# Performance work log

Measured on AMD Instinct MI355X. Metric: run time of the kernel, lower is better.

## Reference

```python
import jax, jax.numpy as jnp
import numpy as np
from jax import lax

DIM = 1024
B, N = 4, 4096


def setup_inputs() -> dict:
    key = jax.random.key(0)
    k1, k2 = jax.random.split(key)
    x = jax.random.normal(k1, (B, N, DIM), dtype=jnp.float32)
    # Linear(dim, 3*dim, bias=False): weight stored as [3*dim, dim] (torch convention)
    w_qkva = jax.random.normal(k2, (3 * DIM, DIM), dtype=jnp.float32) * (DIM ** -0.5)
    gamma = jnp.ones((DIM,), dtype=jnp.float32)  # RMSNorm gain
    return {"x": x, "w_qkva": w_qkva, "gamma": gamma}


def _rmsnorm(x, gamma):
    # lucidrains RMSNorm: F.normalize(x, dim=-1) * sqrt(dim) * gamma
    scale = jnp.asarray(x.shape[-1], x.dtype) ** 0.5
    norm = jnp.sqrt(jnp.sum(x * x, axis=-1, keepdims=True))
    return x / jnp.maximum(norm, 1e-12) * scale * gamma


def reference(x, w_qkva, gamma):
    h = _rmsnorm(x, gamma)                                  # [b, n, d]
    qkva = jnp.einsum('bnd,ed->bne', h, w_qkva)             # [b, n, 3d]
    q, kv, a = jnp.split(qkva, 3, axis=-1)                  # each [b, n, d]
    a = jax.nn.sigmoid(a)

    def binary_operator(e_i, e_j):
        a_i, kv_i = e_i
        a_j, kv_j = e_j
        return (a_j * a_i, a_j * kv_i + kv_j)

    # gated linear recurrence over the sequence axis (elementwise per channel)
    _, y = lax.associative_scan(binary_operator, (a, kv), axis=1)
    return q * y                                            # [b, n, d]
```

## Files before the change

kernel.cpp:

```cpp
#include <hip/hip_runtime.h>
#include <hip/hip_bf16.h>

#define SEQ_N 4096
#define BATCH 4
#define DIM 1024
#define M_ROWS (BATCH * SEQ_N)
#define NCOLS (3 * DIM)
#define KDIM DIM
#define CHUNK_L 16
#define NCHUNK (SEQ_N / CHUNK_L)
#define NCHANNEL (BATCH * DIM)

using short8 = __attribute__((ext_vector_type(8))) short;
using f32x4  = __attribute__((ext_vector_type(4))) float;

static __device__ __forceinline__ unsigned short f2bf(float f) {
    union { float f; unsigned u; } v; v.f = f;
    unsigned r = v.u + 0x7fffu + ((v.u >> 16) & 1u);
    return (unsigned short)(r >> 16);
}
static __device__ __forceinline__ float bf2f(unsigned short s) {
    union { unsigned u; float f; } v; v.u = ((unsigned)s) << 16;
    return v.f;
}

__global__ __launch_bounds__(256) void prep_kernel(const float* __restrict__ x,
                                                   const float* __restrict__ gamma,
                                                   unsigned short* __restrict__ h,
                                                   const float* __restrict__ w,
                                                   unsigned short* __restrict__ wb) {
    if (blockIdx.x < 4096) {
        const int wave = threadIdx.x >> 6;
        const int lane = threadIdx.x & 63;
        const int row = blockIdx.x * 4 + wave;
        const float4* xr = reinterpret_cast<const float4*>(x + (size_t)row * DIM);
        const float4* gr = reinterpret_cast<const float4*>(gamma);
        float4 v[4];
        float ss = 0.f;
#pragma unroll
        for (int i = 0; i < 4; ++i) {
            v[i] = xr[i * 64 + lane];
            ss += v[i].x * v[i].x + v[i].y * v[i].y + v[i].z * v[i].z + v[i].w * v[i].w;
        }
#pragma unroll
        for (int off = 32; off >= 1; off >>= 1) ss += __shfl_xor(ss, off, 64);
        const float scale = 32.0f / fmaxf(sqrtf(ss), 1e-12f);
        ushort4* hr = reinterpret_cast<ushort4*>(h + (size_t)row * DIM);
#pragma unroll
        for (int i = 0; i < 4; ++i) {
            float4 g = gr[i * 64 + lane];
            ushort4 o;
            o.x = f2bf(v[i].x * scale * g.x);
            o.y = f2bf(v[i].y * scale * g.y);
            o.z = f2bf(v[i].z * scale * g.z);
            o.w = f2bf(v[i].w * scale * g.w);
            hr[i * 64 + lane] = o;
        }
    } else {
        const int i = (blockIdx.x - 4096) * 256 + threadIdx.x;
        float4 vv = reinterpret_cast<const float4*>(w)[i];
        ushort4 o;
        o.x = f2bf(vv.x); o.y = f2bf(vv.y); o.z = f2bf(vv.z); o.w = f2bf(vv.w);
        reinterpret_cast<ushort4*>(wb)[i] = o;
    }
}

__global__ __launch_bounds__(256) void gemm_bt_kernel(const unsigned short* __restrict__ A,
                                                      const unsigned short* __restrict__ B,
                                                      unsigned short* __restrict__ C) {
    __shared__ __align__(16) unsigned short sA[128 * 32];
    __shared__ __align__(16) unsigned short sB[128 * 32];

    const int tid  = threadIdx.x;
    const int lane = tid & 63;
    const int wave = tid >> 6;
    const int row0 = blockIdx.y * 128;
    const int col0 = blockIdx.x * 128;
    const int wm = (wave >> 1) * 64;
    const int wn = (wave & 1) * 64;
    const int fr = lane & 15;
    const int kq = lane >> 4;

    const unsigned short* agp = A + (size_t)(row0 + (tid >> 2)) * KDIM + (tid & 3) * 8;
    const unsigned short* bgp = B + (size_t)(col0 + (tid >> 2)) * KDIM + (tid & 3) * 8;

    f32x4 acc[4][4] = {};

    for (int k0 = 0; k0 < KDIM; k0 += 32) {
        __builtin_amdgcn_global_load_lds(
            (const __attribute__((address_space(1))) void*)(agp),
            (__attribute__((address_space(3))) void*)(&sA[tid * 8]), 16, 0, 0);
        __builtin_amdgcn_global_load_lds(
            (const __attribute__((address_space(1))) void*)(agp + 64 * KDIM),
            (__attribute__((address_space(3))) void*)(&sA[2048 + tid * 8]), 16, 0, 0);
        __builtin_amdgcn_global_load_lds(
            (const __attribute__((address_space(1))) void*)(bgp),
            (__attribute__((address_space(3))) void*)(&sB[tid * 8]), 16, 0, 0);
        __builtin_amdgcn_global_load_lds(
            (const __attribute__((address_space(1))) void*)(bgp + 64 * KDIM),
            (__attribute__((address_space(3))) void*)(&sB[2048 + tid * 8]), 16, 0, 0);
        agp += 32; bgp += 32;
        __syncthreads();

        short8 af[4], bf[4];
#pragma unroll
        for (int i = 0; i < 4; ++i)
            af[i] = *reinterpret_cast<const short8*>(&sA[(wm + i * 16 + fr) * 32 + kq * 8]);
#pragma unroll
        for (int j = 0; j < 4; ++j)
            bf[j] = *reinterpret_cast<const short8*>(&sB[(wn + j * 16 + fr) * 32 + kq * 8]);
#pragma unroll
        for (int i = 0; i < 4; ++i)
#pragma unroll
            for (int j = 0; j < 4; ++j)
                acc[i][j] = __builtin_amdgcn_mfma_f32_16x16x32_bf16(af[i], bf[j], acc[i][j], 0, 0, 0);
        __syncthreads();
    }

#pragma unroll
    for (int i = 0; i < 4; ++i) {
#pragma unroll
        for (int j = 0; j < 4; ++j) {
#pragma unroll
            for (int r = 0; r < 4; ++r) {
                int row = row0 + wm + i * 16 + kq * 4 + r;
                int col = col0 + wn + j * 16 + fr;
                C[(size_t)row * NCOLS + col] = f2bf(acc[i][j][r]);
            }
        }
    }
}

__global__ __launch_bounds__(256) void chunk_agg_kernel(const unsigned short* __restrict__ qkva,
                                                        float2* __restrict__ AY) {
    const int c = blockIdx.x, b = blockIdx.y;
    const int d4 = threadIdx.x;
    const unsigned short* base = qkva + ((size_t)b * SEQ_N + c * CHUNK_L) * NCOLS;
    float s[4] = {0.f, 0.f, 0.f, 0.f};
    float A[4] = {1.f, 1.f, 1.f, 1.f};
#pragma unroll 4
    for (int n = 0; n < CHUNK_L; ++n) {
        ushort4 kv4 = reinterpret_cast<const ushort4*>(base + (size_t)n * NCOLS + DIM)[d4];
        ushort4 av4 = reinterpret_cast<const ushort4*>(base + (size_t)n * NCOLS + 2 * DIM)[d4];
        float kv[4] = {bf2f(kv4.x), bf2f(kv4.y), bf2f(kv4.z), bf2f(kv4.w)};
        float av[4] = {bf2f(av4.x), bf2f(av4.y), bf2f(av4.z), bf2f(av4.w)};
#pragma unroll
        for (int t = 0; t < 4; ++t) {
            float a = 1.f / (1.f + __expf(-av[t]));
            s[t] = a * s[t] + kv[t];
            A[t] *= a;
        }
    }
    float4* o = reinterpret_cast<float4*>(AY + (size_t)c * NCHANNEL + b * DIM);
    float4 p0, p1;
    p0.x = A[0]; p0.y = s[0]; p0.z = A[1]; p0.w = s[1];
    p1.x = A[2]; p1.y = s[2]; p1.z = A[3]; p1.w = s[3];
    o[2 * d4]     = p0;
    o[2 * d4 + 1] = p1;
}

__global__ __launch_bounds__(64) void agg_scan_kernel(const float2* __restrict__ AY,
                                                      float* __restrict__ Sin) {
    const int ch = blockIdx.x * 64 + threadIdx.x;
    float s = 0.f;
#pragma unroll 8
    for (int c = 0; c < NCHUNK; ++c) {
        Sin[(size_t)c * NCHANNEL + ch] = s;
        float2 ay = AY[(size_t)c * NCHANNEL + ch];
        s = ay.x * s + ay.y;
    }
}

__global__ __launch_bounds__(256) void apply_kernel(const unsigned short* __restrict__ qkva,
                                                    const float* __restrict__ Sin,
                                                    float* __restrict__ out) {
    const int c = blockIdx.x, b = blockIdx.y;
    const int d4 = threadIdx.x;
    const unsigned short* base = qkva + ((size_t)b * SEQ_N + c * CHUNK_L) * NCOLS;
    float* obase = out + ((size_t)b * SEQ_N + c * CHUNK_L) * DIM;
    float4 s4 = reinterpret_cast<const float4*>(Sin + (size_t)c * NCHANNEL + b * DIM)[d4];
    float s[4] = {s4.x, s4.y, s4.z, s4.w};
#pragma unroll 4
    for (int n = 0; n < CHUNK_L; ++n) {
        ushort4 kv4 = reinterpret_cast<const ushort4*>(base + (size_t)n * NCOLS + DIM)[d4];
        ushort4 av4 = reinterpret_cast<const ushort4*>(base + (size_t)n * NCOLS + 2 * DIM)[d4];
        ushort4 q4  = reinterpret_cast<const ushort4*>(base + (size_t)n * NCOLS)[d4];
        float kv[4] = {bf2f(kv4.x), bf2f(kv4.y), bf2f(kv4.z), bf2f(kv4.w)};
        float av[4] = {bf2f(av4.x), bf2f(av4.y), bf2f(av4.z), bf2f(av4.w)};
        float q[4]  = {bf2f(q4.x),  bf2f(q4.y),  bf2f(q4.z),  bf2f(q4.w)};
        float4 o;
        {
            float a0 = 1.f / (1.f + __expf(-av[0])); s[0] = a0 * s[0] + kv[0]; o.x = q[0] * s[0];
            float a1 = 1.f / (1.f + __expf(-av[1])); s[1] = a1 * s[1] + kv[1]; o.y = q[1] * s[1];
            float a2 = 1.f / (1.f + __expf(-av[2])); s[2] = a2 * s[2] + kv[2]; o.z = q[2] * s[2];
            float a3 = 1.f / (1.f + __expf(-av[3])); s[3] = a3 * s[3] + kv[3]; o.w = q[3] * s[3];
        }
        reinterpret_cast<float4*>(obase + (size_t)n * DIM)[d4] = o;
    }
}

extern "C" void kernel_launch(void* const* d_in, const int* in_sizes, int n_in,
                              void* d_out, int out_size, void* d_ws, size_t ws_size,
                              hipStream_t stream) {
    const float* x     = (const float*)d_in[0];
    const float* w     = (const float*)d_in[1];
    const float* gamma = (const float*)d_in[2];
    float* out = (float*)d_out;

    char* ws = (char*)d_ws;
    unsigned short* wb   = (unsigned short*)(ws);
    unsigned short* h    = (unsigned short*)(ws + 6291456);
    unsigned short* qkva = (unsigned short*)(ws + 39845888);
    float2* AY  = (float2*)(ws + 6291456);
    float*  Sin = (float*)(ws + 6291456 + 8388608);

    prep_kernel<<<4096 + 3072, 256, 0, stream>>>(x, gamma, h, w, wb);
    gemm_bt_kernel<<<dim3(NCOLS / 128, M_ROWS / 128), 256, 0, stream>>>(h, wb, qkva);
    chunk_agg_kernel<<<dim3(NCHUNK, BATCH), 256, 0, stream>>>(qkva, AY);
    agg_scan_kernel<<<NCHANNEL / 64, 64, 0, stream>>>(AY, Sin);
    apply_kernel<<<dim3(NCHUNK, BATCH), 256, 0, stream>>>(qkva, Sin, out);
}
```

Measured before the change: 302.5 us.

## Fuse chunk aggregation, carry scan and apply into one cooperative kernel

Replaces the three separate scan kernels with one cooperative kernel of 512 blocks. Each block handles two chunk/batch tiles per phase, and the phases are separated by grid-wide syncs. The intent is to remove two kernel launches and their inter-kernel gaps. In exchange it adds two grid.sync barriers and runs the serial carry scan on only 16 blocks of 256 threads, which may spread that latency-bound phase across fewer CUs than before.

```diff
diff --git a/kernel.cpp b/kernel.cpp
--- a/kernel.cpp
+++ b/kernel.cpp
@@ -1,5 +1,8 @@
 #include <hip/hip_runtime.h>
 #include <hip/hip_bf16.h>
+#include <hip/hip_cooperative_groups.h>
+
+namespace cg = cooperative_groups;
 
 #define SEQ_N 4096
 #define BATCH 4
@@ -131,71 +134,81 @@
     }
 }
 
-__global__ __launch_bounds__(256) void chunk_agg_kernel(const unsigned short* __restrict__ qkva,
-                                                        float2* __restrict__ AY) {
-    const int c = blockIdx.x, b = blockIdx.y;
-    const int d4 = threadIdx.x;
-    const unsigned short* base = qkva + ((size_t)b * SEQ_N + c * CHUNK_L) * NCOLS;
-    float s[4] = {0.f, 0.f, 0.f, 0.f};
-    float A[4] = {1.f, 1.f, 1.f, 1.f};
+__global__ __launch_bounds__(256) void fused_scan_kernel(const unsigned short* __restrict__ qkva,
+                                                         float2* __restrict__ AY,
+                                                         float* __restrict__ Sin,
+                                                         float* __restrict__ out) {
+    cg::grid_group grid = cg::this_grid();
+    const int tid = threadIdx.x;
+
+#pragma unroll
+    for (int pp = 0; pp < 2; ++pp) {
+        const int p = blockIdx.x + pp * 512;
+        const int c = p & 255, b = p >> 8;
+        const unsigned short* base = qkva + ((size_t)b * SEQ_N + c * CHUNK_L) * NCOLS;
+        float s[4] = {0.f, 0.f, 0.f, 0.f};
+        float A[4] = {1.f, 1.f, 1.f, 1.f};
 #pragma unroll 4
-    for (int n = 0; n < CHUNK_L; ++n) {
-        ushort4 kv4 = reinterpret_cast<const ushort4*>(base + (size_t)n * NCOLS + DIM)[d4];
-        ushort4 av4 = reinterpret_cast<const ushort4*>(base + (size_t)n * NCOLS + 2 * DIM)[d4];
-        float kv[4] = {bf2f(kv4.x), bf2f(kv4.y), bf2f(kv4.z), bf2f(kv4.w)};
-        float av[4] = {bf2f(av4.x), bf2f(av4.y), bf2f(av4.z), bf2f(av4.w)};
-#pragma unroll
-        for (int t = 0; t < 4; ++t) {
-            float a = 1.f / (1.f + __expf(-av[t]));
-            s[t] = a * s[t] + kv[t];
-            A[t] *= a;
-        }
-    }
-    float4* o = reinterpret_cast<float4*>(AY + (size_t)c * NCHANNEL + b * DIM);
-    float4 p0, p1;
-    p0.x = A[0]; p0.y = s[0]; p0.z = A[1]; p0.w = s[1];
-    p1.x = A[2]; p1.y = s[2]; p1.z = A[3]; p1.w = s[3];
-    o[2 * d4]     = p0;
-    o[2 * d4 + 1] = p1;
-}
-
-__global__ __launch_bounds__(64) void agg_scan_kernel(const float2* __restrict__ AY,
-                                                      float* __restrict__ Sin) {
-    const int ch = blockIdx.x * 64 + threadIdx.x;
-    float s = 0.f;
+        for (int n = 0; n < CHUNK_L; ++n) {
+            ushort4 kv4 = reinterpret_cast<const ushort4*>(base + (size_t)n * NCOLS + DIM)[tid];
+            ushort4 av4 = reinterpret_cast<const ushort4*>(base + (size_t)n * NCOLS + 2 * DIM)[tid];
+            float kv[4] = {bf2f(kv4.x), bf2f(kv4.y), bf2f(kv4.z), bf2f(kv4.w)};
+            float av[4] = {bf2f(av4.x), bf2f(av4.y), bf2f(av4.z), bf2f(av4.w)};
+#pragma unroll
+            for (int t = 0; t < 4; ++t) {
+                float a = 1.f / (1.f + __expf(-av[t]));
+                s[t] = a * s[t] + kv[t];
+                A[t] *= a;
+            }
+        }
+        float4* o = reinterpret_cast<float4*>(AY + (size_t)c * NCHANNEL + b * DIM);
+        float4 p0, p1;
+        p0.x = A[0]; p0.y = s[0]; p0.z = A[1]; p0.w = s[1];
+        p1.x = A[2]; p1.y = s[2]; p1.z = A[3]; p1.w = s[3];
+        o[2 * tid]     = p0;
+        o[2 * tid + 1] = p1;
+    }
+
+    grid.sync();
+
+    if (blockIdx.x < 16) {
+        const int ch = blockIdx.x * 256 + tid;
+        float s = 0.f;
 #pragma unroll 8
-    for (int c = 0; c < NCHUNK; ++c) {
-        Sin[(size_t)c * NCHANNEL + ch] = s;
-        float2 ay = AY[(size_t)c * NCHANNEL + ch];
-        s = ay.x * s + ay.y;
-    }
-}
-
-__global__ __launch_bounds__(256) void apply_kernel(const unsigned short* __restrict__ qkva,
-                                                    const float* __restrict__ Sin,
-                                                    float* __restrict__ out) {
-    const int c = blockIdx.x, b = blockIdx.y;
-    const int d4 = threadIdx.x;
-    const unsigned short* base = qkva + ((size_t)b * SEQ_N + c * CHUNK_L) * NCOLS;
-    float* obase = out + ((size_t)b * SEQ_N + c * CHUNK_L) * DIM;
-    float4 s4 = reinterpret_cast<const float4*>(Sin + (size_t)c * NCHANNEL + b * DIM)[d4];
-    float s[4] = {s4.x, s4.y, s4.z, s4.w};
+        for (int c = 0; c < NCHUNK; ++c) {
+            Sin[(size_t)c * NCHANNEL + ch] = s;
+            float2 ay = AY[(size_t)c * NCHANNEL + ch];
+            s = ay.x * s + ay.y;
+        }
+    }
+
+    grid.sync();
+
+#pragma unroll
+    for (int pp = 0; pp < 2; ++pp) {
+        const int p = blockIdx.x + pp * 512;
+        const int c = p & 255, b = p >> 8;
+        const unsigned short* base = qkva + ((size_t)b * SEQ_N + c * CHUNK_L) * NCOLS;
+        float* obase = out + ((size_t)b * SEQ_N + c * CHUNK_L) * DIM;
+        float4 s4 = reinterpret_cast<const float4*>(Sin + (size_t)c * NCHANNEL + b * DIM)[tid];
+        float s[4] = {s4.x, s4.y, s4.z, s4.w};
 #pragma unroll 4
-    for (int n = 0; n < CHUNK_L; ++n) {
-        ushort4 kv4 = reinterpret_cast<const ushort4*>(base + (size_t)n * NCOLS + DIM)[d4];
-        ushort4 av4 = reinterpret_cast<const ushort4*>(base + (size_t)n * NCOLS + 2 * DIM)[d4];
-        ushort4 q4  = reinterpret_cast<const ushort4*>(base + (size_t)n * NCOLS)[d4];
-        float kv[4] = {bf2f(kv4.x), bf2f(kv4.y), bf2f(kv4.z), bf2f(kv4.w)};
-        float av[4] = {bf2f(av4.x), bf2f(av4.y), bf2f(av4.z), bf2f(av4.w)};
-        float q[4]  = {bf2f(q4.x),  bf2f(q4.y),  bf2f(q4.z),  bf2f(q4.w)};
-        float4 o;
-        {
-            float a0 = 1.f / (1.f + __expf(-av[0])); s[0] = a0 * s[0] + kv[0]; o.x = q[0] * s[0];
-            float a1 = 1.f / (1.f + __expf(-av[1])); s[1] = a1 * s[1] + kv[1]; o.y = q[1] * s[1];
-            float a2 = 1.f / (1.f + __expf(-av[2])); s[2] = a2 * s[2] + kv[2]; o.z = q[2] * s[2];
-            float a3 = 1.f / (1.f + __expf(-av[3])); s[3] = a3 * s[3] + kv[3]; o.w = q[3] * s[3];
-        }
-        reinterpret_cast<float4*>(obase + (size_t)n * DIM)[d4] = o;
+        for (int n = 0; n < CHUNK_L; ++n) {
+            ushort4 kv4 = reinterpret_cast<const ushort4*>(base + (size_t)n * NCOLS + DIM)[tid];
+            ushort4 av4 = reinterpret_cast<const ushort4*>(base + (size_t)n * NCOLS + 2 * DIM)[tid];
+            ushort4 q4  = reinterpret_cast<const ushort4*>(base + (size_t)n * NCOLS)[tid];
+            float kv[4] = {bf2f(kv4.x), bf2f(kv4.y), bf2f(kv4.z), bf2f(kv4.w)};
+            float av[4] = {bf2f(av4.x), bf2f(av4.y), bf2f(av4.z), bf2f(av4.w)};
+            float q[4]  = {bf2f(q4.x),  bf2f(q4.y),  bf2f(q4.z),  bf2f(q4.w)};
+            float4 o;
+            {
+                float a0 = 1.f / (1.f + __expf(-av[0])); s[0] = a0 * s[0] + kv[0]; o.x = q[0] * s[0];
+                float a1 = 1.f / (1.f + __expf(-av[1])); s[1] = a1 * s[1] + kv[1]; o.y = q[1] * s[1];
+                float a2 = 1.f / (1.f + __expf(-av[2])); s[2] = a2 * s[2] + kv[2]; o.z = q[2] * s[2];
+                float a3 = 1.f / (1.f + __expf(-av[3])); s[3] = a3 * s[3] + kv[3]; o.w = q[3] * s[3];
+            }
+            reinterpret_cast<float4*>(obase + (size_t)n * DIM)[tid] = o;
+        }
     }
 }
 
@@ -216,7 +229,8 @@
 
     prep_kernel<<<4096 + 3072, 256, 0, stream>>>(x, gamma, h, w, wb);
     gemm_bt_kernel<<<dim3(NCOLS / 128, M_ROWS / 128), 256, 0, stream>>>(h, wb, qkva);
-    chunk_agg_kernel<<<dim3(NCHUNK, BATCH), 256, 0, stream>>>(qkva, AY);
-    agg_scan_kernel<<<NCHANNEL / 64, 64, 0, stream>>>(AY, Sin);
-    apply_kernel<<<dim3(NCHUNK, BATCH), 256, 0, stream>>>(qkva, Sin, out);
-}
+
+    void* args[] = {(void*)&qkva, (void*)&AY, (void*)&Sin, (void*)&out};
+    hipLaunchCooperativeKernel((void*)fused_scan_kernel, dim3(512), dim3(256),
+                               args, 0, stream);
+}
```

New measurement: 419.8 us. 38.8% more time.
